# Kernel optimization log

Measured on AMD Instinct MI355X. Metric: run time of the kernel, lower is better.

## Reference

```python
import jax, jax.numpy as jnp
import numpy as np

D_ATTN = 2048
D_STATE = 64
SHIFT_FRAC = 0.5
LN_EPS = 1e-5


def setup_inputs() -> dict:
    key = jax.random.key(0)
    ks = jax.random.split(key, 8)
    B, T = 8, 2048
    s_attn = 1.0 / np.sqrt(D_ATTN)
    s_state = 1.0 / np.sqrt(D_STATE)
    x = jax.random.normal(ks[0], (B, T, D_ATTN), jnp.float32)
    W_key = jax.random.normal(ks[1], (D_STATE, D_ATTN), jnp.float32) * s_attn
    W_value = jax.random.normal(ks[2], (D_STATE, D_ATTN), jnp.float32) * s_attn
    W_output = jax.random.normal(ks[3], (D_ATTN, D_STATE), jnp.float32) * s_state
    W_shift = jax.random.normal(ks[4], (D_ATTN, D_ATTN), jnp.float32) * s_attn
    gate = jnp.ones((D_ATTN,), jnp.float32)
    # negative decay log so w = exp(time_decay) in (e^-1, 1): stable over T=2048 steps
    time_decay = -jax.random.uniform(ks[5], (D_STATE,), jnp.float32, 0.05, 1.0)
    time_first = jax.random.normal(ks[6], (D_STATE,), jnp.float32) * 0.1
    ln_gamma = jnp.ones((D_ATTN,), jnp.float32)
    ln_beta = jnp.zeros((D_ATTN,), jnp.float32)
    return dict(x=x, W_key=W_key, W_value=W_value, W_output=W_output,
                W_shift=W_shift, gate=gate, time_decay=time_decay,
                time_first=time_first, ln_gamma=ln_gamma, ln_beta=ln_beta)


def reference(x, W_key, W_value, W_output, W_shift, gate, time_decay,
              time_first, ln_gamma, ln_beta):
    B, T, D = x.shape
    # token shift: cat([x[:, s:], x[:, :-s]], dim=1) == roll(x, -s, axis=1)
    shift_len = max(1, int(T * SHIFT_FRAC))
    x_cat = jnp.roll(x, -shift_len, axis=1)
    g = jax.nn.sigmoid(gate)
    x_shift = jnp.einsum('btd,ed->bte', x_cat, W_shift) * g + x * (1.0 - g)
    # LayerNorm over last dim
    mu = jnp.mean(x_shift, axis=-1, keepdims=True)
    var = jnp.var(x_shift, axis=-1, keepdims=True)
    x_norm = (x_shift - mu) * jax.lax.rsqrt(var + LN_EPS) * ln_gamma + ln_beta
    k = jnp.einsum('btd,sd->bts', x_norm, W_key)    # (B,T,Ds)
    v = jnp.einsum('btd,sd->bts', x_norm, W_value)  # (B,T,Ds)
    w = jnp.exp(time_decay)                          # (Ds,)
    u = jnp.exp(time_first)                          # (Ds,)
    wkv = jnp.exp(-u * jax.nn.sigmoid(k)) * v        # (B,T,Ds)
    # linear recurrence: state_t = w * state_{t-1} + wkv_t
    def step(state, wkv_t):
        state = state * w + wkv_t
        return state, state
    init = jnp.zeros((B, k.shape[-1]), x.dtype)
    last_state, states = jax.lax.scan(step, init, jnp.swapaxes(wkv, 0, 1))
    states = jnp.swapaxes(states, 0, 1)              # (B,T,Ds)
    # per-step output projection == single batched GEMM over stacked states
    output = jnp.einsum('bts,ds->btd', states, W_output)  # (B,T,D)
    # dropout in eval mode is identity; last_state is detached in original
    return output, jax.lax.stop_gradient(last_state)
```

## Files before the change

### kernel.cpp

```cpp
#include <hip/hip_runtime.h>
#include <stdint.h>

constexpr int kD  = 2048;
constexpr int kDS = 64;
constexpr int kNT = 2048;
constexpr int kM  = 8 * kNT;
constexpr int kOutElems = kM * kD;

typedef __attribute__((ext_vector_type(8))) short short8;
typedef __attribute__((ext_vector_type(8))) unsigned short bfu8;
typedef __attribute__((ext_vector_type(4))) float f32x4;

__device__ __forceinline__ unsigned short f2bf(float f) {
  unsigned int u = __float_as_uint(f);
  return (unsigned short)((u + 0x7FFFu + ((u >> 16) & 1u)) >> 16);
}
__device__ __forceinline__ float bf2f(unsigned short b) {
  return __uint_as_float(((unsigned int)b) << 16);
}

__device__ __forceinline__ void gload16(const void* g, void* l) {
  __builtin_amdgcn_global_load_lds((__attribute__((address_space(1))) void*)g,
                                   (__attribute__((address_space(3))) void*)l,
                                   16, 0, 0);
}

__global__ void k_cvt(const float* __restrict__ src, unsigned short* __restrict__ dst, int n8) {
  int i8 = blockIdx.x * 256 + threadIdx.x;
  if (i8 >= n8) return;
  const f32x4* s = (const f32x4*)(src + (size_t)i8 * 8);
  f32x4 v0 = s[0], v1 = s[1];
  bfu8 o;
  o[0] = f2bf(v0[0]); o[1] = f2bf(v0[1]); o[2] = f2bf(v0[2]); o[3] = f2bf(v0[3]);
  o[4] = f2bf(v1[0]); o[5] = f2bf(v1[1]); o[6] = f2bf(v1[2]); o[7] = f2bf(v1[3]);
  *(bfu8*)(dst + (size_t)i8 * 8) = o;
}

__launch_bounds__(256)
__global__ void k_cvt_kv_g(const float* __restrict__ wk, const float* __restrict__ wv,
                           const float* __restrict__ gamma, const float* __restrict__ beta,
                           unsigned short* __restrict__ dst, float2* __restrict__ cgb) {
  int b = blockIdx.x;
  int tid = threadIdx.x;
  int s = b >> 1;
  const float* src = (b & 1) ? wv : wk;
  int d0 = tid * 8;
  const f32x4* p = (const f32x4*)(src + (size_t)s * kD + d0);
  f32x4 v0 = p[0], v1 = p[1];
  f32x4 g0 = *(const f32x4*)&gamma[d0], g1 = *(const f32x4*)&gamma[d0 + 4];
  f32x4 b0 = *(const f32x4*)&beta[d0],  b1 = *(const f32x4*)&beta[d0 + 4];
  bfu8 o;
  float sg = 0.f, sb = 0.f;
#pragma unroll
  for (int j = 0; j < 4; ++j) {
    float gw0 = g0[j] * v0[j], gw1 = g1[j] * v1[j];
    o[j] = f2bf(gw0); o[j + 4] = f2bf(gw1);
    sg += gw0 + gw1;
    sb += b0[j] * v0[j] + b1[j] * v1[j];
  }
  *(bfu8*)(dst + (size_t)b * kD + d0) = o;
#pragma unroll
  for (int d = 1; d < 64; d <<= 1) { sg += __shfl_xor(sg, d); sb += __shfl_xor(sb, d); }
  __shared__ float gg[4], bb[4];
  if ((tid & 63) == 0) { gg[tid >> 6] = sg; bb[tid >> 6] = sb; }
  __syncthreads();
  if (tid == 0)
    cgb[b] = make_float2(gg[0] + gg[1] + gg[2] + gg[3], bb[0] + bb[1] + bb[2] + bb[3]);
}

#define MM(x,y,z) __builtin_amdgcn_mfma_f32_16x16x32_bf16(x,y,z,0,0,0)
#define BAR __builtin_amdgcn_s_barrier()
#define WAITV_(N) asm volatile("s_waitcnt vmcnt(" #N ")" ::: "memory")
#define WAITV(N) WAITV_(N)
#define WAITL asm volatile("s_waitcnt lgkmcnt(0)")
#define NOWV (void)0

#define STAGEA_TO(BUF,H,Q,KT) gload16(aS + (size_t)(((H)*64+(Q)*128)*2048) + (KT), \
                                      smem + (BUF)*32768 + ((H)*64+(Q)*128)*64 + ldsAst)
#define STAGEB_TO(BUF,H,Q,KT) gload16(bS + (size_t)(((H)*32+(Q)*128)*2048) + (KT), \
                                      smem + (BUF)*32768 + 16384 + (H)*2048 + (Q)*8192 + ldsBst)

#define RDA(CUR,H,MF,KS) (*(const short8*)(smem + (CUR)*32768 + ardb + (H)*4096 + (MF)*1024 + colrd##KS))
#define RDB(CUR,H,NF,KS) (*(const short8*)(smem + (CUR)*32768 + 16384 + brdb + (H)*2048 + (NF)*1024 + colrd##KS))

#define RD_A(CUR,H) \
  a[0][0]=RDA(CUR,H,0,0); a[0][1]=RDA(CUR,H,0,1); \
  a[1][0]=RDA(CUR,H,1,0); a[1][1]=RDA(CUR,H,1,1); \
  a[2][0]=RDA(CUR,H,2,0); a[2][1]=RDA(CUR,H,2,1); \
  a[3][0]=RDA(CUR,H,3,0); a[3][1]=RDA(CUR,H,3,1)
#define RD_B(CUR,H,BV) \
  BV[0][0]=RDB(CUR,H,0,0); BV[0][1]=RDB(CUR,H,0,1); \
  BV[1][0]=RDB(CUR,H,1,0); BV[1][1]=RDB(CUR,H,1,1)

#define MF16(MH, B, NB) \
  __builtin_amdgcn_s_setprio(1); \
  acc[(MH)*4+0][(NB)+0] = MM(a[0][0], B[0][0], acc[(MH)*4+0][(NB)+0]); \
  acc[(MH)*4+0][(NB)+1] = MM(a[0][0], B[1][0], acc[(MH)*4+0][(NB)+1]); \
  acc[(MH)*4+1][(NB)+0] = MM(a[1][0], B[0][0], acc[(MH)*4+1][(NB)+0]); \
  acc[(MH)*4+1][(NB)+1] = MM(a[1][0], B[1][0], acc[(MH)*4+1][(NB)+1]); \
  acc[(MH)*4+2][(NB)+0] = MM(a[2][0], B[0][0], acc[(MH)*4+2][(NB)+0]); \
  acc[(MH)*4+2][(NB)+1] = MM(a[2][0], B[1][0], acc[(MH)*4+2][(NB)+1]); \
  acc[(MH)*4+3][(NB)+0] = MM(a[3][0], B[0][0], acc[(MH)*4+3][(NB)+0]); \
  acc[(MH)*4+3][(NB)+1] = MM(a[3][0], B[1][0], acc[(MH)*4+3][(NB)+1]); \
  acc[(MH)*4+0][(NB)+0] = MM(a[0][1], B[0][1], acc[(MH)*4+0][(NB)+0]); \
  acc[(MH)*4+0][(NB)+1] = MM(a[0][1], B[1][1], acc[(MH)*4+0][(NB)+1]); \
  acc[(MH)*4+1][(NB)+0] = MM(a[1][1], B[0][1], acc[(MH)*4+1][(NB)+0]); \
  acc[(MH)*4+1][(NB)+1] = MM(a[1][1], B[1][1], acc[(MH)*4+1][(NB)+1]); \
  acc[(MH)*4+2][(NB)+0] = MM(a[2][1], B[0][1], acc[(MH)*4+2][(NB)+0]); \
  acc[(MH)*4+2][(NB)+1] = MM(a[2][1], B[1][1], acc[(MH)*4+2][(NB)+1]); \
  acc[(MH)*4+3][(NB)+0] = MM(a[3][1], B[0][1], acc[(MH)*4+3][(NB)+0]); \
  acc[(MH)*4+3][(NB)+1] = MM(a[3][1], B[1][1], acc[(MH)*4+3][(NB)+1]); \
  __builtin_amdgcn_s_setprio(0)

#define PH0(CUR, S, KA1, WV) \
  BAR; WAITL; MF16(0, b0, 0); \
  RD_B(CUR,1,b1); \
  if (S) { STAGEA_TO((CUR)^1, 1, 0, KA1); STAGEA_TO((CUR)^1, 1, 1, KA1); } \
  WV

#define PH1(CUR, S, KT2, WV) \
  BAR; WAITL; MF16(0, b1, 2); \
  RD_A(CUR,1); \
  if (S) { STAGEA_TO(CUR, 0, 0, KT2); STAGEA_TO(CUR, 0, 1, KT2); } \
  WV

#define PH2(CUR, S, KT2, WV) \
  BAR; WAITL; MF16(1, b0, 0); \
  if (S) { STAGEB_TO(CUR, 0, 0, KT2); STAGEB_TO(CUR, 0, 1, KT2); } \
  WV

#define PH3(CUR, RDN, S, KT2, WV) \
  BAR; WAITL; MF16(1, b1, 2); \
  if (RDN) { RD_A((CUR)^1,0); RD_B((CUR)^1,0,b0); } \
  if (S) { STAGEB_TO(CUR, 1, 0, KT2); STAGEB_TO(CUR, 1, 1, KT2); } \
  WV

__global__ __launch_bounds__(512, 2)
void k_gemm_shift8(const unsigned short* __restrict__ A,
                   const unsigned short* __restrict__ Bw,
                   const float* __restrict__ gate,
                   unsigned short* __restrict__ out) {
  __shared__ __align__(16) unsigned char smem_raw[131072];
  unsigned short* smem = (unsigned short*)smem_raw;

  const int tid = threadIdx.x;
  const int lane = tid & 63;
  const int w = tid >> 6;
  const int wr = w >> 2, wc = w & 3;
  const int lr = lane & 15, lq = lane >> 4;
  const int bid = blockIdx.x;
  const int nblk = bid & 7, mblk = bid >> 3;
  const int m0 = mblk * 256, n0 = nblk * 256;

  const int r0 = tid >> 3;
  const int colel = ((tid & 7) * 8) ^ (((tid >> 3) & 7) << 3);
  const unsigned short* aS = A + (size_t)((m0 ^ 1024) + r0) * 2048 + colel;
  const unsigned short* bS = Bw + (size_t)(n0 + ((tid >> 8) << 6) + (r0 & 31)) * 2048 + colel;
  const int ldsAst = tid * 8;
  const int ldsBst = ((tid >> 8) << 12) + (tid & 255) * 8;

  const int ardb = (wr * 128 + lr) * 64;
  const int brdb = (wc * 64 + lr) * 64;
  const int colrd0 = (lq * 8) ^ ((lr & 7) << 3);
  const int colrd1 = (32 + lq * 8) ^ ((lr & 7) << 3);

  short8 a[4][2], b0[2][2], b1[2][2];
  f32x4 acc[8][4] = {};

  STAGEA_TO(0,0,0,0); STAGEA_TO(0,0,1,0);
  STAGEB_TO(0,0,0,0); STAGEB_TO(0,0,1,0);
  STAGEB_TO(0,1,0,0); STAGEB_TO(0,1,1,0);
  STAGEA_TO(0,1,0,0); STAGEA_TO(0,1,1,0);
  STAGEA_TO(1,0,0,64); STAGEA_TO(1,0,1,64);
  STAGEB_TO(1,0,0,64); STAGEB_TO(1,0,1,64);
  STAGEB_TO(1,1,0,64); STAGEB_TO(1,1,1,64);
  WAITV(6); BAR;
  RD_A(0,0); RD_B(0,0,b0);

  int ka1 = 64, kt2 = 128;
  for (int j = 0; j < 15; ++j) {
    PH0(0, 1, ka1, WAITV(8)); PH1(0, 1, kt2, WAITV(8));
    PH2(0, 1, kt2, WAITV(8)); PH3(0, 1, 1, kt2, WAITV(8));
    ka1 += 64; kt2 += 64;
    PH0(1, 1, ka1, WAITV(8)); PH1(1, 1, kt2, WAITV(8));
    PH2(1, 1, kt2, WAITV(8)); PH3(1, 1, 1, kt2, WAITV(8));
    ka1 += 64; kt2 += 64;
  }
  PH0(0, 1, 1984, WAITV(8)); PH1(0, 0, 0, NOWV);
  PH2(0, 0, 0, WAITV(4));    PH3(0, 1, 0, 0, WAITV(2));
  PH0(1, 0, 0, WAITV(0));    PH1(1, 0, 0, NOWV);
  PH2(1, 0, 0, NOWV);        PH3(1, 0, 0, 0, NOWV);

  float* cbuf = (float*)smem_raw;
#pragma unroll
  for (int q = 0; q < 4; ++q) {
    __syncthreads();
    if (wr == (q >> 1)) {
#pragma unroll
      for (int mm = 0; mm < 4; ++mm) {
#pragma unroll
        for (int nf = 0; nf < 4; ++nf) {
#pragma unroll
          for (int i = 0; i < 4; ++i) {
            int rl = mm * 16 + lq * 4 + i;
            int cl = wc * 64 + nf * 16 + lr;
            cbuf[rl * 260 + cl] = acc[(q & 1) * 4 + mm][nf][i];
          }
        }
      }
    }
    __syncthreads();
#pragma unroll
    for (int it = 0; it < 4; ++it) {
      int idx = tid + it * 512;
      int rl = idx >> 5, cb = (idx & 31) * 8;
      int gr = m0 + q * 64 + rl, gc = n0 + cb;
      f32x4 c0 = *(const f32x4*)&cbuf[rl * 260 + cb];
      f32x4 c1 = *(const f32x4*)&cbuf[rl * 260 + cb + 4];
      f32x4 g0 = *(const f32x4*)&gate[gc];
      f32x4 g1 = *(const f32x4*)&gate[gc + 4];
      bfu8 xv = *(const bfu8*)(A + (size_t)gr * 2048 + gc);
      bfu8 o;
#pragma unroll
      for (int jj = 0; jj < 4; ++jj) {
        float g = 1.f / (1.f + __expf(-g0[jj]));
        o[jj] = f2bf(c0[jj] * g + bf2f(xv[jj]) * (1.f - g));
        float h = 1.f / (1.f + __expf(-g1[jj]));
        o[jj + 4] = f2bf(c1[jj] * h + bf2f(xv[jj + 4]) * (1.f - h));
      }
      *(bfu8*)(out + (size_t)gr * 2048 + gc) = o;
    }
  }
}

__launch_bounds__(256)
__global__ void k_stats(const unsigned short* __restrict__ xs, float2* __restrict__ stats) {
  int m = blockIdx.x;
  int tid = threadIdx.x;
  bfu8 v = *(const bfu8*)(xs + (size_t)m * kD + tid * 8);
  float s = 0.f, q = 0.f;
#pragma unroll
  for (int j = 0; j < 8; ++j) { float f = bf2f(v[j]); s += f; q += f * f; }
#pragma unroll
  for (int d = 1; d < 64; d <<= 1) { s += __shfl_xor(s, d); q += __shfl_xor(q, d); }
  __shared__ float ss[4], qq[4];
  if ((tid & 63) == 0) { ss[tid >> 6] = s; qq[tid >> 6] = q; }
  __syncthreads();
  if (tid == 0) {
    s = ss[0] + ss[1] + ss[2] + ss[3];
    q = qq[0] + qq[1] + qq[2] + qq[3];
    float mean = s * (1.f / kD);
    float var = q * (1.f / kD) - mean * mean;
    stats[m] = make_float2(mean, rsqrtf(var + 1e-5f));
  }
}

__launch_bounds__(256, 2)
__global__ void k_gemm_kv_f(const unsigned short* __restrict__ A,
                            const unsigned short* __restrict__ Bw,
                            const float2* __restrict__ stats,
                            const float2* __restrict__ cgb,
                            const float* __restrict__ tfirst,
                            float* __restrict__ wkv) {
  __shared__ __align__(16) unsigned short As[32 * 32];
  __shared__ __align__(16) unsigned short Bs[128 * 32];
  __shared__ float2 rowst[32];
  const int tid = threadIdx.x;
  const int lane = tid & 63;
  const int wcv = tid >> 6;
  const int m0 = blockIdx.x * 32;
  const int lr = lane & 15, lk = (lane >> 4) << 3;
  const int c1 = tid, c2 = tid + 256;

  if (tid < 32) rowst[tid] = stats[m0 + tid];

  const unsigned short* ga = A + (size_t)(m0 + (tid >> 2)) * kD + ((tid & 3) << 3);
  const unsigned short* gb0 = Bw + (size_t)(c1 >> 2) * kD + ((c1 & 3) << 3);
  const unsigned short* gb1 = Bw + (size_t)(c2 >> 2) * kD + ((c2 & 3) << 3);
  unsigned short* la = As + tid * 8;
  unsigned short* lb0 = Bs + c1 * 8;
  unsigned short* lb1 = Bs + c2 * 8;

  f32x4 acc[2][2] = {};

  for (int kt = 0; kt < kD; kt += 32) {
    __syncthreads();
    if (tid < 128) gload16(ga + kt, la);
    gload16(gb0 + kt, lb0);
    gload16(gb1 + kt, lb1);
    __syncthreads();
    short8 af[2], bf[2];
#pragma unroll
    for (int mf = 0; mf < 2; ++mf)
      af[mf] = *(const short8*)&As[(mf * 16 + lr) * 32 + lk];
#pragma unroll
    for (int nf = 0; nf < 2; ++nf)
      bf[nf] = *(const short8*)&Bs[(wcv * 32 + nf * 16 + lr) * 32 + lk];
#pragma unroll
    for (int mf = 0; mf < 2; ++mf)
#pragma unroll
      for (int nf = 0; nf < 2; ++nf)
        acc[mf][nf] = __builtin_amdgcn_mfma_f32_16x16x32_bf16(af[mf], bf[nf], acc[mf][nf], 0, 0, 0);
  }

  const int fq = lane >> 4, fr = lane & 15;
#pragma unroll
  for (int mf = 0; mf < 2; ++mf) {
#pragma unroll
    for (int nf = 0; nf < 2; ++nf) {
      int c = wcv * 32 + nf * 16 + fr;
      float2 gc = cgb[c];
#pragma unroll
      for (int i = 0; i < 4; ++i) {
        int rloc = mf * 16 + fq * 4 + i;
        float2 st = rowst[rloc];
        float val = st.y * (acc[mf][nf][i] - st.x * gc.x) + gc.y;
        float other = __shfl_xor(val, 1);
        if (!(c & 1)) {
          int s = c >> 1;
          float sk = 1.f / (1.f + expf(-val));
          float u = expf(tfirst[s]);
          wkv[(size_t)(m0 + rloc) * kDS + s] = expf(-u * sk) * other;
        }
      }
    }
  }
}

__global__ void k_scan(const float* __restrict__ wkv, const float* __restrict__ tdec,
                       unsigned short* __restrict__ states, float* __restrict__ last_state) {
  int chunk = blockIdx.x;
  int b = blockIdx.y;
  int s = threadIdx.x;
  float w = expf(tdec[s]);
  int t1 = chunk * 64;
  int warm = t1 < 256 ? t1 : 256;
  const float* base = wkv + (size_t)b * kNT * kDS + s;
  unsigned short* sbase = states + (size_t)b * kNT * kDS + s;
  float st = 0.f;
#pragma unroll 4
  for (int t = t1 - warm; t < t1; ++t) st = fmaf(st, w, base[(size_t)t * kDS]);
#pragma unroll 4
  for (int t = t1; t < t1 + 64; ++t) {
    st = fmaf(st, w, base[(size_t)t * kDS]);
    sbase[(size_t)t * kDS] = f2bf(st);
  }
  if (chunk == 31) last_state[b * kDS + s] = st;
}

__launch_bounds__(256, 3)
__global__ void k_out_gemm(const unsigned short* __restrict__ states,
                           const unsigned short* __restrict__ Wo,
                           float* __restrict__ out) {
  __shared__ __align__(16) unsigned char sraw[33792];
  unsigned short* As = (unsigned short*)sraw;
  unsigned short* Bs = As + 8192;
  float* cbuf = (float*)sraw;
  const int tid = threadIdx.x;
  const int lane = tid & 63;
  const int w = tid >> 6;
  const int wr = w >> 1, wc = w & 1;
  const int lr = lane & 15, lq = lane >> 4;
  const int n0 = blockIdx.x * 128;
  const int m0 = blockIdx.y * 128;

  const int sr0 = tid >> 3;
  const int scol = ((tid & 7) * 8) ^ (((tid >> 3) & 7) << 3);
#pragma unroll
  for (int rd = 0; rd < 4; ++rd) {
    gload16(states + (size_t)(m0 + sr0 + rd * 32) * 64 + scol, As + tid * 8 + rd * 2048);
    gload16(Wo + (size_t)(n0 + sr0 + rd * 32) * 64 + scol, Bs + tid * 8 + rd * 2048);
  }
  __syncthreads();

  short8 a[4][2], b[4][2];
#pragma unroll
  for (int mf = 0; mf < 4; ++mf) {
#pragma unroll
    for (int ks = 0; ks < 2; ++ks) {
      int col = (ks * 32 + lq * 8) ^ ((lr & 7) << 3);
      a[mf][ks] = *(const short8*)&As[(wr * 64 + mf * 16 + lr) * 64 + col];
      b[mf][ks] = *(const short8*)&Bs[(wc * 64 + mf * 16 + lr) * 64 + col];
    }
  }
  f32x4 acc[4][4] = {};
#pragma unroll
  for (int mf = 0; mf < 4; ++mf)
#pragma unroll
    for (int nf = 0; nf < 4; ++nf) {
      acc[mf][nf] = __builtin_amdgcn_mfma_f32_16x16x32_bf16(a[mf][0], b[nf][0], acc[mf][nf], 0, 0, 0);
      acc[mf][nf] = __builtin_amdgcn_mfma_f32_16x16x32_bf16(a[mf][1], b[nf][1], acc[mf][nf], 0, 0, 0);
    }

#pragma unroll
  for (int q = 0; q < 2; ++q) {
    __syncthreads();
    if (wr == q) {
#pragma unroll
      for (int mf = 0; mf < 4; ++mf)
#pragma unroll
        for (int nf = 0; nf < 4; ++nf)
#pragma unroll
          for (int i = 0; i < 4; ++i) {
            int rl = mf * 16 + lq * 4 + i;
            int cl = wc * 64 + nf * 16 + lr;
            cbuf[rl * 132 + cl] = acc[mf][nf][i];
          }
    }
    __syncthreads();
#pragma unroll
    for (int it = 0; it < 8; ++it) {
      int idx = tid + it * 256;
      int rl = idx >> 5, cb = (idx & 31) * 4;
      *(f32x4*)&out[(size_t)(m0 + q * 64 + rl) * kD + n0 + cb] = *(const f32x4*)&cbuf[rl * 132 + cb];
    }
  }
}

extern "C" void kernel_launch(void* const* d_in, const int* in_sizes, int n_in,
                              void* d_out, int out_size, void* d_ws, size_t ws_size,
                              hipStream_t stream) {
  const float* x    = (const float*)d_in[0];
  const float* Wk   = (const float*)d_in[1];
  const float* Wv   = (const float*)d_in[2];
  const float* Wo   = (const float*)d_in[3];
  const float* Wsh  = (const float*)d_in[4];
  const float* gate = (const float*)d_in[5];
  const float* tdec = (const float*)d_in[6];
  const float* tfir = (const float*)d_in[7];
  const float* lng  = (const float*)d_in[8];
  const float* lnb  = (const float*)d_in[9];
  float* out = (float*)d_out;
  char* ws = (char*)d_ws;

  unsigned short* xbf   = (unsigned short*)(ws);
  unsigned short* wshbf = (unsigned short*)(ws + 67108864);
  unsigned short* wkvbf = (unsigned short*)(ws + 75497472);
  float* wkvf           = (float*)(ws + 76021760);
  unsigned short* stbf  = (unsigned short*)(ws + 80216064);
  unsigned short* wobf  = (unsigned short*)(ws + 82313216);
  float2* statsp        = (float2*)(ws + 82575360);
  float2* cgbp          = (float2*)(ws + 82706432);

  k_cvt<<<16384, 256, 0, stream>>>(x, xbf, 4194304);
  k_cvt<<<2048, 256, 0, stream>>>(Wsh, wshbf, 524288);
  k_cvt<<<64, 256, 0, stream>>>(Wo, wobf, 16384);
  k_cvt_kv_g<<<128, 256, 0, stream>>>(Wk, Wv, lng, lnb, wkvbf, cgbp);

  k_gemm_shift8<<<512, 512, 0, stream>>>(xbf, wshbf, gate, (unsigned short*)out);
  k_stats<<<16384, 256, 0, stream>>>((const unsigned short*)out, statsp);
  k_gemm_kv_f<<<512, 256, 0, stream>>>((const unsigned short*)out, wkvbf, statsp, cgbp, tfir, wkvf);
  k_scan<<<dim3(32, 8), 64, 0, stream>>>(wkvf, tdec, stbf, out + kOutElems);
  k_out_gemm<<<dim3(16, 128), 256, 0, stream>>>(stbf, wobf, out);
}
```

Measured before the change: 275.5 us.

## Restructure shift GEMM k-loop into per-tile phases with two barriers each

Reorganizes the double-buffered main loop of the bf16 shift GEMM. Each k-tile now runs four phases that issue their LDS fragment reads and global-to-LDS stages before the MFMA block, with barriers on both sides. The prefetch order and vmcnt thresholds are rearranged to match. The aim is better overlap of LDS reads and global prefetch with MFMA work, at the cost of twice as many barriers and a more delicate buffer-reuse ordering.

```diff
diff --git a/kernel.cpp b/kernel.cpp
--- a/kernel.cpp
+++ b/kernel.cpp
@@ -73,6 +73,7 @@
 #define WAITV_(N) asm volatile("s_waitcnt vmcnt(" #N ")" ::: "memory")
 #define WAITV(N) WAITV_(N)
 #define WAITL asm volatile("s_waitcnt lgkmcnt(0)")
+#define WAITL8 asm volatile("s_waitcnt lgkmcnt(8)")
 #define NOWV (void)0
 
 #define STAGEA_TO(BUF,H,Q,KT) gload16(aS + (size_t)(((H)*64+(Q)*128)*2048) + (KT), \
@@ -112,28 +113,27 @@
   acc[(MH)*4+3][(NB)+1] = MM(a[3][1], B[1][1], acc[(MH)*4+3][(NB)+1]); \
   __builtin_amdgcn_s_setprio(0)
 
-#define PH0(CUR, S, KA1, WV) \
-  BAR; WAITL; MF16(0, b0, 0); \
+#define QH0(CUR, SB1, KB1) \
+  RD_A(CUR,0); RD_B(CUR,0,b0); \
+  if (SB1) { STAGEB_TO((CUR)^1,1,0,KB1); STAGEB_TO((CUR)^1,1,1,KB1); } \
+  WAITL8; BAR; WAITL; MF16(0, b0, 0); BAR
+
+#define QH1(CUR, SA, KT2) \
   RD_B(CUR,1,b1); \
-  if (S) { STAGEA_TO((CUR)^1, 1, 0, KA1); STAGEA_TO((CUR)^1, 1, 1, KA1); } \
-  WV
-
-#define PH1(CUR, S, KT2, WV) \
-  BAR; WAITL; MF16(0, b1, 2); \
+  if (SA) { STAGEA_TO(CUR,0,0,KT2); STAGEA_TO(CUR,0,1,KT2); } \
+  BAR; WAITL; MF16(0, b1, 2); BAR
+
+#define QH2(CUR) \
   RD_A(CUR,1); \
-  if (S) { STAGEA_TO(CUR, 0, 0, KT2); STAGEA_TO(CUR, 0, 1, KT2); } \
-  WV
-
-#define PH2(CUR, S, KT2, WV) \
-  BAR; WAITL; MF16(1, b0, 0); \
-  if (S) { STAGEB_TO(CUR, 0, 0, KT2); STAGEB_TO(CUR, 0, 1, KT2); } \
-  WV
-
-#define PH3(CUR, RDN, S, KT2, WV) \
-  BAR; WAITL; MF16(1, b1, 2); \
-  if (RDN) { RD_A((CUR)^1,0); RD_B((CUR)^1,0,b0); } \
-  if (S) { STAGEB_TO(CUR, 1, 0, KT2); STAGEB_TO(CUR, 1, 1, KT2); } \
-  WV
+  BAR; WAITL; MF16(1, b0, 0); BAR
+
+#define QH3(CUR, SA, KT2, WV) \
+  if (SA) { STAGEA_TO(CUR,1,0,KT2); STAGEA_TO(CUR,1,1,KT2); \
+            STAGEB_TO(CUR,0,0,KT2); STAGEB_TO(CUR,0,1,KT2); } \
+  BAR; WAITL; MF16(1, b1, 2); WV; BAR
+
+#define KTILE(CUR, KB1, KT2, SB1, SA, WV) \
+  QH0(CUR, SB1, KB1); QH1(CUR, SA, KT2); QH2(CUR); QH3(CUR, SA, KT2, WV)
 
 __global__ __launch_bounds__(512, 2)
 void k_gemm_shift8(const unsigned short* __restrict__ A,
@@ -168,28 +168,21 @@
   f32x4 acc[8][4] = {};
 
   STAGEA_TO(0,0,0,0); STAGEA_TO(0,0,1,0);
+  STAGEA_TO(0,1,0,0); STAGEA_TO(0,1,1,0);
   STAGEB_TO(0,0,0,0); STAGEB_TO(0,0,1,0);
   STAGEB_TO(0,1,0,0); STAGEB_TO(0,1,1,0);
-  STAGEA_TO(0,1,0,0); STAGEA_TO(0,1,1,0);
   STAGEA_TO(1,0,0,64); STAGEA_TO(1,0,1,64);
+  STAGEA_TO(1,1,0,64); STAGEA_TO(1,1,1,64);
   STAGEB_TO(1,0,0,64); STAGEB_TO(1,0,1,64);
-  STAGEB_TO(1,1,0,64); STAGEB_TO(1,1,1,64);
   WAITV(6); BAR;
-  RD_A(0,0); RD_B(0,0,b0);
-
-  int ka1 = 64, kt2 = 128;
+
+  int kb1 = 64, kt2 = 128;
   for (int j = 0; j < 15; ++j) {
-    PH0(0, 1, ka1, WAITV(8)); PH1(0, 1, kt2, WAITV(8));
-    PH2(0, 1, kt2, WAITV(8)); PH3(0, 1, 1, kt2, WAITV(8));
-    ka1 += 64; kt2 += 64;
-    PH0(1, 1, ka1, WAITV(8)); PH1(1, 1, kt2, WAITV(8));
-    PH2(1, 1, kt2, WAITV(8)); PH3(1, 1, 1, kt2, WAITV(8));
-    ka1 += 64; kt2 += 64;
-  }
-  PH0(0, 1, 1984, WAITV(8)); PH1(0, 0, 0, NOWV);
-  PH2(0, 0, 0, WAITV(4));    PH3(0, 1, 0, 0, WAITV(2));
-  PH0(1, 0, 0, WAITV(0));    PH1(1, 0, 0, NOWV);
-  PH2(1, 0, 0, NOWV);        PH3(1, 0, 0, 0, NOWV);
+    KTILE(0, kb1, kt2, 1, 1, WAITV(6)); kb1 += 64; kt2 += 64;
+    KTILE(1, kb1, kt2, 1, 1, WAITV(6)); kb1 += 64; kt2 += 64;
+  }
+  KTILE(0, 1984, 0, 1, 0, WAITV(0));
+  KTILE(1, 0, 0, 0, 0, NOWV);
 
   float* cbuf = (float*)smem_raw;
 #pragma unroll
```

New measurement: 282.6 us. 1.03x slower.
